# Optimization experiments

Measured on AMD Instinct MI355X. Metric: run time of the kernel, lower is better.

Reference implementation:

```python
import jax, jax.numpy as jnp
import numpy as np

B, H, W = 8, 512, 512
KSIZE = 11   # HVS Gaussian kernel size
SIGMA = 2.0
EPS = 1e-8


def _gauss_kernel():
    ax = jnp.arange(KSIZE, dtype=jnp.float32) - (KSIZE - 1) / 2.0
    g = jnp.exp(-(ax ** 2) / (2.0 * SIGMA ** 2))
    k = jnp.outer(g, g)
    return k / jnp.sum(k)


def _conv_same(x, k):
    # x: (B,1,H,W), k: (kh,kw) symmetric -> conv == correlation
    return jax.lax.conv_general_dilated(
        x, k[None, None, :, :], window_strides=(1, 1), padding='SAME',
        dimension_numbers=('NCHW', 'OIHW', 'NCHW'))


def setup_inputs() -> dict:
    key = jax.random.key(0)
    k1, k2, k3 = jax.random.split(key, 3)
    prob_map = jax.random.uniform(k1, (B, 1, H, W), dtype=jnp.float32,
                                  minval=0.01, maxval=0.99)
    c = jax.random.uniform(k2, (B, 1, H, W), dtype=jnp.float32)
    # binary halftone sampled per-pixel from prob_map
    h_sampled = (jax.random.uniform(k3, (B, 1, H, W)) < prob_map).astype(jnp.float32)
    return {"prob_map": prob_map, "c": c, "h_sampled": h_sampled}


def reference(prob_map, c, h_sampled):
    k = _gauss_kernel()
    # perceived error of the sampled halftone: e = G*h - c
    e = _conv_same(h_sampled, k) - c                     # (B,1,H,W)
    corr = _conv_same(e, k)                              # (G*e), G symmetric
    sum_k2 = jnp.sum(k * k)
    delta = 1.0 - 2.0 * h_sampled                        # flip change per pixel
    # reward_calc.compute_reward_with_flip, vectorized over all pixels:
    # E(flip at a) - E = 2*delta_a*(G*e)(a) + delta_a^2 * sum(G^2)
    reward = 2.0 * delta * corr + (delta ** 2) * sum_k2  # >0 means flip hurts
    log_prob = jnp.where(h_sampled > 0.5,
                         jnp.log(prob_map + EPS),
                         jnp.log(1.0 - prob_map + EPS))
    # local expected-gradient (REINFORCE) loss, averaged over batch
    loss = -jnp.sum(reward * log_prob) / prob_map.shape[0]
    return loss
```

## Files before the change

kernel.cpp:

```cpp
#include <hip/hip_runtime.h>

typedef float v2f __attribute__((ext_vector_type(2)));
typedef float v4f __attribute__((ext_vector_type(4)));

#define IMG 512
#define TS  32
#define TPB 2
#define NBLK 1024

#define A_STR  56
#define BT_STR 46
#define E_STR  44
#define CT_STR 34

#define HQUADS 728

__device__ __forceinline__ v2f lo2(v4f v) { return __builtin_shufflevector(v, v, 0, 1); }
__device__ __forceinline__ v2f hi2(v4f v) { return __builtin_shufflevector(v, v, 2, 3); }

__device__ __forceinline__ v4f ldq(const float* __restrict__ hmap, size_t base,
                                   int x0, int y0, int idx) {
    int r = idx / 14, q = idx - r * 14;
    int gy = y0 - 10 + r, gx0 = x0 - 12 + 4 * q;
    v4f v = {0.f, 0.f, 0.f, 0.f};
    if ((unsigned)gy < IMG) {
        const float* hr = &hmap[base + ((size_t)gy << 9)];
        if (gx0 >= 0 && gx0 + 3 < IMG) {
            v = *(const v4f*)&hr[gx0];
        } else {
            if ((unsigned)(gx0 + 0) < IMG) v.x = hr[gx0 + 0];
            if ((unsigned)(gx0 + 1) < IMG) v.y = hr[gx0 + 1];
            if ((unsigned)(gx0 + 2) < IMG) v.z = hr[gx0 + 2];
            if ((unsigned)(gx0 + 3) < IMG) v.w = hr[gx0 + 3];
        }
    }
    return v;
}

__global__ __launch_bounds__(256, 4) void marl_fused(
    const float* __restrict__ prob,
    const float* __restrict__ cmap,
    const float* __restrict__ hmap,
    float* __restrict__ out)
{
    __shared__ __align__(16) float Abuf[52 * A_STR];
    __shared__ __align__(16) float Bbuf[56 * BT_STR];
    __shared__ float red[4];

    const float W[11] = {0.00881223f, 0.02714358f, 0.06511405f, 0.12164908f,
                         0.17699840f, 0.20056540f, 0.17699840f, 0.12164908f,
                         0.06511405f, 0.02714358f, 0.00881223f};
    v2f wv[11];
#pragma unroll
    for (int i = 0; i < 11; ++i) wv[i] = (v2f){W[i], W[i]};
    float w2 = 0.f;
#pragma unroll
    for (int i = 0; i < 11; ++i) w2 += W[i] * W[i];
    const float sumk2 = w2 * w2;
    const v2f z = {0.f, 0.f};

    const int tid = threadIdx.x;
    const int i0 = tid, i1 = tid + 256, i2 = tid + 512;
    const int T0 = blockIdx.x * TPB;

    {
        int b = T0 >> 8, r8 = T0 & 255;
        int x0 = (r8 & 15) * TS, y0 = (r8 >> 4) * TS;
        size_t base = (size_t)b << 18;
        v4f a = ldq(hmap, base, x0, y0, i0);
        v4f bq = ldq(hmap, base, x0, y0, i1);
        v4f c = (tid < 216) ? ldq(hmap, base, x0, y0, i2) : (v4f){0.f,0.f,0.f,0.f};
        { int r = i0 / 14, q = i0 - r * 14; *(v4f*)&Abuf[r * A_STR + 4 * q] = a; }
        { int r = i1 / 14, q = i1 - r * 14; *(v4f*)&Abuf[r * A_STR + 4 * q] = bq; }
        if (tid < 216) { int r = i2 / 14, q = i2 - r * 14; *(v4f*)&Abuf[r * A_STR + 4 * q] = c; }
    }
    __syncthreads();

    float partial = 0.f;

    for (int t = 0; t < TPB; ++t) {
        const int T = T0 + t;
        const int b = T >> 8, r8 = T & 255;
        const int x0 = (r8 & 15) * TS, y0 = (r8 >> 4) * TS;
        const size_t base = (size_t)b << 18;

        if (tid < 196) {
            int q = tid % 14, run = tid / 14;
            int by0 = 3 * run;
            v2f accLo[3] = {z, z, z}, accHi[3] = {z, z, z};
#pragma unroll
            for (int i = 0; i < 13; ++i) {
                v4f a = *(const v4f*)&Abuf[(by0 + i) * A_STR + 4 * q];
                v2f lo = lo2(a), hi = hi2(a);
#pragma unroll
                for (int r = 0; r < 3; ++r) {
                    int j = i - r;
                    if (j >= 0 && j < 11) { accLo[r] += wv[j] * lo; accHi[r] += wv[j] * hi; }
                }
            }
#pragma unroll
            for (int r = 0; r < 3; ++r) {
                int by = by0 + r;
                Bbuf[(4 * q + 0) * BT_STR + by] = accLo[r].x;
                Bbuf[(4 * q + 1) * BT_STR + by] = accLo[r].y;
                Bbuf[(4 * q + 2) * BT_STR + by] = accHi[r].x;
                Bbuf[(4 * q + 3) * BT_STR + by] = accHi[r].y;
            }
        }
        __syncthreads();

        if (tid < 231) {
            int eq = tid % 11, p = tid / 11;
            int ex0 = 4 * eq, ey0 = 2 * p;
            v2f acc[4] = {z, z, z, z};
#pragma unroll
            for (int i = 0; i < 14; ++i) {
                v2f bb = *(const v2f*)&Bbuf[(ex0 + 2 + i) * BT_STR + ey0];
#pragma unroll
                for (int c = 0; c < 4; ++c) {
                    int j = i - c;
                    if (j >= 0 && j < 11) acc[c] += wv[j] * bb;
                }
            }
#pragma unroll
            for (int c = 0; c < 4; ++c) {
                int ex = ex0 + c;
                if (ex < 42) {
                    int gx = x0 - 5 + ex;
                    bool xin = (unsigned)gx < IMG;
#pragma unroll
                    for (int h = 0; h < 2; ++h) {
                        int gy = y0 - 5 + ey0 + h;
                        float v = 0.f;
                        if (xin && (unsigned)gy < IMG)
                            v = acc[c][h] - cmap[base + ((size_t)gy << 9) + gx];
                        Abuf[(ey0 + h) * E_STR + ex] = v;
                    }
                }
            }
        }
        __syncthreads();

        v4f pf0, pf1, pf2;
        const bool havepf = (t + 1 < TPB);
        int nx0 = 0, ny0 = 0; size_t nbase = 0;
        if (havepf) {
            int Tn = T + 1;
            int nb = Tn >> 8, nr8 = Tn & 255;
            nx0 = (nr8 & 15) * TS; ny0 = (nr8 >> 4) * TS;
            nbase = (size_t)nb << 18;
            pf0 = ldq(hmap, nbase, nx0, ny0, i0);
            pf1 = ldq(hmap, nbase, nx0, ny0, i1);
            if (tid < 216) pf2 = ldq(hmap, nbase, nx0, ny0, i2);
        }
        if (tid < 176) {
            int eq = tid % 11, run = tid / 11;
            int ex0 = 4 * eq, oy0 = 2 * run;
            v2f accLo[2] = {z, z}, accHi[2] = {z, z};
#pragma unroll
            for (int i = 0; i < 12; ++i) {
                v4f e = *(const v4f*)&Abuf[(oy0 + i) * E_STR + ex0];
                v2f lo = lo2(e), hi = hi2(e);
#pragma unroll
                for (int r = 0; r < 2; ++r) {
                    int j = i - r;
                    if (j >= 0 && j < 11) { accLo[r] += wv[j] * lo; accHi[r] += wv[j] * hi; }
                }
            }
#pragma unroll
            for (int r = 0; r < 2; ++r) {
                int oy = oy0 + r;
                Bbuf[(ex0 + 0) * CT_STR + oy] = accLo[r].x;
                Bbuf[(ex0 + 1) * CT_STR + oy] = accLo[r].y;
                if (ex0 + 2 < 42) {
                    Bbuf[(ex0 + 2) * CT_STR + oy] = accHi[r].x;
                    Bbuf[(ex0 + 3) * CT_STR + oy] = accHi[r].y;
                }
            }
        }
        __syncthreads();

        if (havepf) {
            { int r = i0 / 14, q = i0 - r * 14; *(v4f*)&Abuf[r * A_STR + 4 * q] = pf0; }
            { int r = i1 / 14, q = i1 - r * 14; *(v4f*)&Abuf[r * A_STR + 4 * q] = pf1; }
            if (tid < 216) { int r = i2 / 14, q = i2 - r * 14; *(v4f*)&Abuf[r * A_STR + 4 * q] = pf2; }
        }
        {
            int oxh = tid % 16, p = tid / 16;
            int ox0 = 2 * oxh, oy0 = 2 * p;
            v2f acc[2] = {z, z};
#pragma unroll
            for (int i = 0; i < 12; ++i) {
                v2f ct = *(const v2f*)&Bbuf[(ox0 + i) * CT_STR + oy0];
#pragma unroll
                for (int c = 0; c < 2; ++c) {
                    int j = i - c;
                    if (j >= 0 && j < 11) acc[c] += wv[j] * ct;
                }
            }
#pragma unroll
            for (int h = 0; h < 2; ++h) {
                int gy = y0 + oy0 + h;
                size_t rowb = base + ((size_t)gy << 9) + (x0 + ox0);
                v2f hv = *(const v2f*)&hmap[rowb];
                v2f pv = *(const v2f*)&prob[rowb];
#pragma unroll
                for (int c = 0; c < 2; ++c) {
                    float h_ = hv[c], p_ = pv[c];
                    float logp = __logf(h_ > 0.5f ? p_ + 1e-8f : 1.f - p_ + 1e-8f);
                    float delta = 1.f - 2.f * h_;
                    partial += (2.f * delta * acc[c][h] + sumk2) * logp;
                }
            }
        }
        __syncthreads();
    }

#pragma unroll
    for (int off = 32; off > 0; off >>= 1)
        partial += __shfl_down(partial, off, 64);
    if ((tid & 63) == 0) red[tid >> 6] = partial;
    __syncthreads();
    if (tid == 0) {
        float s = red[0] + red[1] + red[2] + red[3];
        atomicAdd(out, s * -0.125f);
    }
}

extern "C" void kernel_launch(void* const* d_in, const int* in_sizes, int n_in,
                              void* d_out, int out_size, void* d_ws, size_t ws_size,
                              hipStream_t stream) {
    const float* prob = (const float*)d_in[0];
    const float* cmap = (const float*)d_in[1];
    const float* hmap = (const float*)d_in[2];
    float* out = (float*)d_out;

    hipMemsetAsync(out, 0, sizeof(float), stream);

    marl_fused<<<dim3(NBLK), dim3(256), 0, stream>>>(prob, cmap, hmap, out);
}
```

Baseline: 93.69 us.

## Stage cmap tile in shared memory and prefetch all global loads early

The target image c is now loaded into a new shared-memory tile (Cbuf) with vectorized coalesced loads at tile start and prefetched for the next tile, instead of scattered scalar global reads inside the E stage. The h and prob values for the final reduction are also loaded up front into registers. Work-item indices are remapped across wavefronts (wk), and the tile loop is unrolled. This is meant to hide global-memory latency behind compute, at the cost of extra shared memory and registers, which may lower occupancy.

```diff
diff --git a/kernel.cpp b/kernel.cpp
--- a/kernel.cpp
+++ b/kernel.cpp
@@ -12,8 +12,7 @@
 #define BT_STR 46
 #define E_STR  44
 #define CT_STR 34
-
-#define HQUADS 728
+#define C_STR  48
 
 __device__ __forceinline__ v2f lo2(v4f v) { return __builtin_shufflevector(v, v, 0, 1); }
 __device__ __forceinline__ v2f hi2(v4f v) { return __builtin_shufflevector(v, v, 2, 3); }
@@ -37,6 +36,25 @@
     return v;
 }
 
+__device__ __forceinline__ v4f ldc(const float* __restrict__ cmap, size_t base,
+                                   int x0, int y0, int idx) {
+    int r = idx / 12, q = idx - r * 12;
+    int gy = y0 - 5 + r, gx0 = x0 - 8 + 4 * q;
+    v4f v = {0.f, 0.f, 0.f, 0.f};
+    if ((unsigned)gy < IMG) {
+        const float* cr = &cmap[base + ((size_t)gy << 9)];
+        if (gx0 >= 0 && gx0 + 3 < IMG) {
+            v = *(const v4f*)&cr[gx0];
+        } else {
+            if ((unsigned)(gx0 + 0) < IMG) v.x = cr[gx0 + 0];
+            if ((unsigned)(gx0 + 1) < IMG) v.y = cr[gx0 + 1];
+            if ((unsigned)(gx0 + 2) < IMG) v.z = cr[gx0 + 2];
+            if ((unsigned)(gx0 + 3) < IMG) v.w = cr[gx0 + 3];
+        }
+    }
+    return v;
+}
+
 __global__ __launch_bounds__(256, 4) void marl_fused(
     const float* __restrict__ prob,
     const float* __restrict__ cmap,
@@ -45,6 +63,7 @@
 {
     __shared__ __align__(16) float Abuf[52 * A_STR];
     __shared__ __align__(16) float Bbuf[56 * BT_STR];
+    __shared__ __align__(16) float Cbuf[42 * C_STR];
     __shared__ float red[4];
 
     const float W[11] = {0.00881223f, 0.02714358f, 0.06511405f, 0.12164908f,
@@ -60,32 +79,48 @@
     const v2f z = {0.f, 0.f};
 
     const int tid = threadIdx.x;
+    const int wk  = (tid & 63) * 4 + (tid >> 6);
     const int i0 = tid, i1 = tid + 256, i2 = tid + 512;
     const int T0 = blockIdx.x * TPB;
 
+    const int ox0 = 2 * (tid & 15), oy0e = 2 * (tid >> 4);
+
+    v2f hv[TPB][2], pv[TPB][2];
+
     {
-        int b = T0 >> 8, r8 = T0 & 255;
-        int x0 = (r8 & 15) * TS, y0 = (r8 >> 4) * TS;
-        size_t base = (size_t)b << 18;
-        v4f a = ldq(hmap, base, x0, y0, i0);
-        v4f bq = ldq(hmap, base, x0, y0, i1);
-        v4f c = (tid < 216) ? ldq(hmap, base, x0, y0, i2) : (v4f){0.f,0.f,0.f,0.f};
-        { int r = i0 / 14, q = i0 - r * 14; *(v4f*)&Abuf[r * A_STR + 4 * q] = a; }
-        { int r = i1 / 14, q = i1 - r * 14; *(v4f*)&Abuf[r * A_STR + 4 * q] = bq; }
-        if (tid < 216) { int r = i2 / 14, q = i2 - r * 14; *(v4f*)&Abuf[r * A_STR + 4 * q] = c; }
+        const int b = T0 >> 8, r8 = T0 & 255;
+        const int x0 = (r8 & 15) * TS, y0 = (r8 >> 4) * TS;
+        const size_t base = (size_t)b << 18;
+        v4f ha = ldq(hmap, base, x0, y0, i0);
+        v4f hb = ldq(hmap, base, x0, y0, i1);
+        v4f hc = (tid < 216) ? ldq(hmap, base, x0, y0, i2) : (v4f){0.f,0.f,0.f,0.f};
+        v4f ca = ldc(cmap, base, x0, y0, i0);
+        v4f cb = (tid < 248) ? ldc(cmap, base, x0, y0, i1) : (v4f){0.f,0.f,0.f,0.f};
+#pragma unroll
+        for (int h = 0; h < 2; ++h) {
+            size_t rowb = base + ((size_t)(y0 + oy0e + h) << 9) + (x0 + ox0);
+            hv[0][h] = *(const v2f*)&hmap[rowb];
+            pv[0][h] = *(const v2f*)&prob[rowb];
+        }
+        { int r = i0 / 14, q = i0 - r * 14; *(v4f*)&Abuf[r * A_STR + 4 * q] = ha; }
+        { int r = i1 / 14, q = i1 - r * 14; *(v4f*)&Abuf[r * A_STR + 4 * q] = hb; }
+        if (tid < 216) { int r = i2 / 14, q = i2 - r * 14; *(v4f*)&Abuf[r * A_STR + 4 * q] = hc; }
+        { int r = i0 / 12, q = i0 - r * 12; *(v4f*)&Cbuf[r * C_STR + 4 * q] = ca; }
+        if (tid < 248) { int r = i1 / 12, q = i1 - r * 12; *(v4f*)&Cbuf[r * C_STR + 4 * q] = cb; }
     }
     __syncthreads();
 
     float partial = 0.f;
-
+    v4f pfh0, pfh1, pfh2, pfc0, pfc1;
+
+#pragma unroll
     for (int t = 0; t < TPB; ++t) {
         const int T = T0 + t;
-        const int b = T >> 8, r8 = T & 255;
+        const int r8 = T & 255;
         const int x0 = (r8 & 15) * TS, y0 = (r8 >> 4) * TS;
-        const size_t base = (size_t)b << 18;
-
-        if (tid < 196) {
-            int q = tid % 14, run = tid / 14;
+
+        if (wk < 196) {
+            int q = wk % 14, run = wk / 14;
             int by0 = 3 * run;
             v2f accLo[3] = {z, z, z}, accHi[3] = {z, z, z};
 #pragma unroll
@@ -109,8 +144,8 @@
         }
         __syncthreads();
 
-        if (tid < 231) {
-            int eq = tid % 11, p = tid / 11;
+        if (wk < 231) {
+            int eq = wk % 11, p = wk / 11;
             int ex0 = 4 * eq, ey0 = 2 * p;
             v2f acc[4] = {z, z, z, z};
 #pragma unroll
@@ -133,7 +168,7 @@
                         int gy = y0 - 5 + ey0 + h;
                         float v = 0.f;
                         if (xin && (unsigned)gy < IMG)
-                            v = acc[c][h] - cmap[base + ((size_t)gy << 9) + gx];
+                            v = acc[c][h] - Cbuf[(ey0 + h) * C_STR + ex + 3];
                         Abuf[(ey0 + h) * E_STR + ex] = v;
                     }
                 }
@@ -141,25 +176,30 @@
         }
         __syncthreads();
 
-        v4f pf0, pf1, pf2;
-        const bool havepf = (t + 1 < TPB);
-        int nx0 = 0, ny0 = 0; size_t nbase = 0;
-        if (havepf) {
-            int Tn = T + 1;
-            int nb = Tn >> 8, nr8 = Tn & 255;
-            nx0 = (nr8 & 15) * TS; ny0 = (nr8 >> 4) * TS;
-            nbase = (size_t)nb << 18;
-            pf0 = ldq(hmap, nbase, nx0, ny0, i0);
-            pf1 = ldq(hmap, nbase, nx0, ny0, i1);
-            if (tid < 216) pf2 = ldq(hmap, nbase, nx0, ny0, i2);
-        }
-        if (tid < 176) {
-            int eq = tid % 11, run = tid / 11;
-            int ex0 = 4 * eq, oy0 = 2 * run;
+        if (t + 1 < TPB) {
+            const int Tn = T + 1;
+            const int nb = Tn >> 8, nr8 = Tn & 255;
+            const int nx0 = (nr8 & 15) * TS, ny0 = (nr8 >> 4) * TS;
+            const size_t nbase = (size_t)nb << 18;
+            pfh0 = ldq(hmap, nbase, nx0, ny0, i0);
+            pfh1 = ldq(hmap, nbase, nx0, ny0, i1);
+            if (tid < 216) pfh2 = ldq(hmap, nbase, nx0, ny0, i2);
+            pfc0 = ldc(cmap, nbase, nx0, ny0, i0);
+            if (tid < 248) pfc1 = ldc(cmap, nbase, nx0, ny0, i1);
+#pragma unroll
+            for (int h = 0; h < 2; ++h) {
+                size_t rowb = nbase + ((size_t)(ny0 + oy0e + h) << 9) + (nx0 + ox0);
+                hv[t + 1][h] = *(const v2f*)&hmap[rowb];
+                pv[t + 1][h] = *(const v2f*)&prob[rowb];
+            }
+        }
+        if (wk < 176) {
+            int eq = wk % 11, run = wk / 11;
+            int ex0 = 4 * eq, oyb = 2 * run;
             v2f accLo[2] = {z, z}, accHi[2] = {z, z};
 #pragma unroll
             for (int i = 0; i < 12; ++i) {
-                v4f e = *(const v4f*)&Abuf[(oy0 + i) * E_STR + ex0];
+                v4f e = *(const v4f*)&Abuf[(oyb + i) * E_STR + ex0];
                 v2f lo = lo2(e), hi = hi2(e);
 #pragma unroll
                 for (int r = 0; r < 2; ++r) {
@@ -169,7 +209,7 @@
             }
 #pragma unroll
             for (int r = 0; r < 2; ++r) {
-                int oy = oy0 + r;
+                int oy = oyb + r;
                 Bbuf[(ex0 + 0) * CT_STR + oy] = accLo[r].x;
                 Bbuf[(ex0 + 1) * CT_STR + oy] = accLo[r].y;
                 if (ex0 + 2 < 42) {
@@ -180,18 +220,18 @@
         }
         __syncthreads();
 
-        if (havepf) {
-            { int r = i0 / 14, q = i0 - r * 14; *(v4f*)&Abuf[r * A_STR + 4 * q] = pf0; }
-            { int r = i1 / 14, q = i1 - r * 14; *(v4f*)&Abuf[r * A_STR + 4 * q] = pf1; }
-            if (tid < 216) { int r = i2 / 14, q = i2 - r * 14; *(v4f*)&Abuf[r * A_STR + 4 * q] = pf2; }
+        if (t + 1 < TPB) {
+            { int r = i0 / 14, q = i0 - r * 14; *(v4f*)&Abuf[r * A_STR + 4 * q] = pfh0; }
+            { int r = i1 / 14, q = i1 - r * 14; *(v4f*)&Abuf[r * A_STR + 4 * q] = pfh1; }
+            if (tid < 216) { int r = i2 / 14, q = i2 - r * 14; *(v4f*)&Abuf[r * A_STR + 4 * q] = pfh2; }
+            { int r = i0 / 12, q = i0 - r * 12; *(v4f*)&Cbuf[r * C_STR + 4 * q] = pfc0; }
+            if (tid < 248) { int r = i1 / 12, q = i1 - r * 12; *(v4f*)&Cbuf[r * C_STR + 4 * q] = pfc1; }
         }
         {
-            int oxh = tid % 16, p = tid / 16;
-            int ox0 = 2 * oxh, oy0 = 2 * p;
             v2f acc[2] = {z, z};
 #pragma unroll
             for (int i = 0; i < 12; ++i) {
-                v2f ct = *(const v2f*)&Bbuf[(ox0 + i) * CT_STR + oy0];
+                v2f ct = *(const v2f*)&Bbuf[(ox0 + i) * CT_STR + oy0e];
 #pragma unroll
                 for (int c = 0; c < 2; ++c) {
                     int j = i - c;
@@ -200,13 +240,9 @@
             }
 #pragma unroll
             for (int h = 0; h < 2; ++h) {
-                int gy = y0 + oy0 + h;
-                size_t rowb = base + ((size_t)gy << 9) + (x0 + ox0);
-                v2f hv = *(const v2f*)&hmap[rowb];
-                v2f pv = *(const v2f*)&prob[rowb];
 #pragma unroll
                 for (int c = 0; c < 2; ++c) {
-                    float h_ = hv[c], p_ = pv[c];
+                    float h_ = hv[t][h][c], p_ = pv[t][h][c];
                     float logp = __logf(h_ > 0.5f ? p_ + 1e-8f : 1.f - p_ + 1e-8f);
                     float delta = 1.f - 2.f * h_;
                     partial += (2.f * delta * acc[c][h] + sumk2) * logp;
```

New measurement: 94.71 us. About the same (+1.1%).
